# Kernel optimization log

Hardware: AMD Instinct MI355X
Metric: run time of the kernel (lower is better)

Reference implementation:

```python
import jax, jax.numpy as jnp
import numpy as np

# ---- static configuration (mirrors TimeFold init + deterministic prepare()) ----
B = 256
F = 512            # fft_length//2 + 1
T = 81             # input STFT frames
WIN = 1022         # window_length == frame_length == fft_length
HOP = 400          # hop_length
SEG = 1000         # segment_length
OVL = 50           # overlap_length
TO_HOP = 100       # deterministic choice of randint(1, hop_size=100)
SIG_LEN = (T - 1) * HOP + WIN            # 33022, inverse_stft output length

# prepare(): t segments kept, gaps of TO_HOP deleted
_t = SIG_LEN // (SEG + TO_HOP)
if SIG_LEN % (SEG + TO_HOP) >= SEG:
    _t += 1                               # _t = 30
KEPT_LEN = _t * SEG                       # 30000
OUT_LEN = SEG + (_t - 1) * (SEG - OVL)    # 28550
NF = 1 + (OUT_LEN - WIN) // HOP           # 69 output STFT frames

# indices kept after deleting the to_hop gaps (complement of delete_indices)
KEEP_IDX = np.concatenate([k * (SEG + TO_HOP) + np.arange(SEG) for k in range(_t)])

# overlap-add blending coefficients (length KEPT_LEN), built exactly as in prepare()
_ramp_up = np.arange(1, OVL + 1, dtype=np.float32) / OVL
_ramp_dn = np.arange(OVL, 0, -1, dtype=np.float32) / OVL
COEFF_INC = np.pad(np.tile(np.pad(_ramp_up, (0, SEG - OVL)), _t - 1), (SEG - OVL, OVL))
COEFF_DEC = np.pad(np.tile(np.pad(_ramp_dn, (SEG - OVL, 0)), _t - 1), (0, SEG))
_c = np.tile(np.pad(np.ones(SEG - 2 * OVL, np.float32), (OVL, OVL)), _t - 2)
_c = np.pad(np.pad(_c, (OVL, 0)), (SEG - OVL, 0), constant_values=1.0)
_c = np.pad(np.pad(_c, (0, OVL)), (0, SEG - OVL), constant_values=1.0)
COEFF_CONST = _c.astype(np.float32)

# final_delete_indices: drop [k*SEG, k*SEG+OVL) for k = 1.._t-1
_mask = np.ones(KEPT_LEN, bool)
for k in range(1, _t):
    _mask[k * SEG:k * SEG + OVL] = False
FINAL_KEEP = np.nonzero(_mask)[0]         # length OUT_LEN

# gather index grids for framing (static)
ISTFT_IDX = np.arange(T)[:, None] * HOP + np.arange(WIN)[None, :]
STFT_IDX = np.arange(NF)[:, None] * HOP + np.arange(WIN)[None, :]


def _hann(n):
    # periodic Hann, matches tf.signal.hann_window(periodic=True)
    return (0.5 - 0.5 * jnp.cos(2.0 * jnp.pi * jnp.arange(n, dtype=jnp.float32) / n)).astype(jnp.float32)


def _synthesis_window():
    w = _hann(WIN)
    denom = w * w
    overlaps = -(-WIN // HOP)
    denom = jnp.pad(denom, (0, overlaps * HOP - WIN))
    denom = denom.reshape(overlaps, HOP).sum(axis=0)
    denom = jnp.tile(denom, overlaps)[:WIN]
    return w / denom


def setup_inputs() -> dict:
    key = jax.random.key(0)
    x = jax.random.normal(key, (B, F, T, 2), dtype=jnp.float32)
    return {"x": x}


def reference(x) -> jnp.ndarray:
    # x: [B, 512, T, 2] real/imag STFT
    stfts = jax.lax.complex(x[..., 0], x[..., 1])          # [B, F, T]
    frames = jnp.transpose(stfts, (0, 2, 1))               # [B, T, F]
    # inverse_stft: irfft each frame, apply synthesis window, overlap-add
    tf_frames = jnp.fft.irfft(frames, n=WIN, axis=-1)
    tf_frames = tf_frames * _synthesis_window()
    sig = jnp.zeros((x.shape[0], SIG_LEN), jnp.float32).at[:, ISTFT_IDX].add(tf_frames)
    # dynamic segment delete (gather of kept indices)
    kept = sig[:, KEEP_IDX]                                # [B, KEPT_LEN]
    # shifted copy: drop first OVL samples, zero-pad at end
    shifted = jnp.concatenate(
        [kept[:, OVL:], jnp.zeros((x.shape[0], OVL), jnp.float32)], axis=1)
    # weighted overlap-add blend
    out = (jnp.asarray(COEFF_CONST) + jnp.asarray(COEFF_DEC)) * kept \
        + jnp.asarray(COEFF_INC) * shifted
    out = out[:, FINAL_KEEP]                               # [B, OUT_LEN]
    # forward STFT (periodic Hann, no padding)
    fr = out[:, STFT_IDX] * _hann(WIN)
    S = jnp.fft.rfft(fr, n=WIN, axis=-1)                   # [B, NF, 512]
    S = jnp.transpose(S, (0, 2, 1))                        # [B, 512, NF]
    return jnp.stack([S.real, S.imag], axis=-1)            # [B, 512, NF, 2]
```

## Files before the change

kernel.cpp:

```cpp
#include <hip/hip_runtime.h>
#include <math.h>

typedef unsigned short u16;
typedef unsigned int u32;

#define B_   256
#define F_   512
#define T_   81
#define WIN_ 1022
#define HOP_ 400
#define NF_  69
#define OUT_LEN_ 28550
#define SEG_ 1000
#define OVL_ 50

#define MA_  20736
#define MB_  17664
#define K_   1024
#define NMA_TILES 162
#define NMB_TILES 138
#define NMA_PAD   168
#define NMB_PAD   144

#define SYNWIN_B   0u
#define HANN_B     4096u
#define BASA_B     8192u
#define BASB_B     (BASA_B + 2097152u)
#define ABUF_B     (BASB_B + 2097152u)
#define TF_B       (ABUF_B + 42467328u)
#define OUTF_B     (TF_B + 42467328u)
#define OUTF_STRIDE_ 28672

typedef __attribute__((ext_vector_type(8))) short bf8_t;
typedef __attribute__((ext_vector_type(4))) float f4_t;
typedef const __attribute__((address_space(1))) void* as1cv;
typedef __attribute__((address_space(3))) void* as3v;

__device__ __forceinline__ float b2f(u16 v) {
  u32 u = ((u32)v) << 16; float f; __builtin_memcpy(&f, &u, 4); return f;
}
__device__ __forceinline__ u16 f2b(float f) {
  u32 u; __builtin_memcpy(&u, &f, 4);
  return (u16)((u + 0x7fffu + ((u >> 16) & 1u)) >> 16);
}

__global__ __launch_bounds__(256) void k1_tables(float* __restrict__ ws) {
  int i = blockIdx.x * 256 + threadIdx.x;
  if (i >= WIN_) return;
  const float twopi_N = 6.283185307179586f / (float)WIN_;
  float w = 0.5f - 0.5f * cosf(twopi_N * (float)i);
  int j = i % HOP_;
  float a = 0.5f - 0.5f * cosf(twopi_N * (float)j);
  float b = 0.5f - 0.5f * cosf(twopi_N * (float)(j + 400));
  float d = a * a + b * b;
  if (j + 800 < WIN_) {
    float c = 0.5f - 0.5f * cosf(twopi_N * (float)(j + 800));
    d += c * c;
  }
  ((float*)((char*)ws + SYNWIN_B))[i] = w / d;
  ((float*)((char*)ws + HANN_B))[i]   = w;
}

__global__ __launch_bounds__(256) void gen_basisA(const float* __restrict__ synwin,
                                                  u16* __restrict__ BA) {
  int n = blockIdx.x;
  float scale = (n < WIN_) ? synwin[n] * (1.0f / (float)WIN_) : 0.f;
  for (int k = threadIdx.x; k < 512; k += 256) {
    int m = (k * n) % WIN_;
    float ang = 6.283185307179586f * (float)m / (float)WIN_;
    float s, c; __sincosf(ang, &s, &c);
    bool edge = (k == 0) || (k == 511);
    float ck = edge ? 1.f : 2.f;
    float re = scale * ck * c;
    float im = edge ? 0.f : -scale * ck * s;
    BA[(size_t)n * K_ + 2 * k]     = f2b(re);
    BA[(size_t)n * K_ + 2 * k + 1] = f2b(im);
  }
}

__global__ __launch_bounds__(256) void gen_basisB(const float* __restrict__ hann,
                                                  u16* __restrict__ BB) {
  int k = blockIdx.x;
  for (int w = threadIdx.x; w < K_; w += 256) {
    float re = 0.f, im = 0.f;
    if (w < WIN_) {
      int m = (k * w) % WIN_;
      float ang = 6.283185307179586f * (float)m / (float)WIN_;
      float s, c; __sincosf(ang, &s, &c);
      float h = hann[w];
      re = h * c; im = -h * s;
    }
    BB[(size_t)(2 * k)     * K_ + w] = f2b(re);
    BB[(size_t)(2 * k + 1) * K_ + w] = f2b(im);
  }
}

__global__ __launch_bounds__(256) void prep1(const float* __restrict__ x,
                                             u16* __restrict__ Abuf) {
  __shared__ float2 tile[32][33];
  int k0 = blockIdx.x * 32, t0 = blockIdx.y * 32, b = blockIdx.z;
  int c = threadIdx.x & 31, rr = threadIdx.x >> 5;
  const float2* xp = (const float2*)x;
#pragma unroll
  for (int i = 0; i < 4; ++i) {
    int k = k0 + rr + 8 * i, t = t0 + c;
    float2 v = make_float2(0.f, 0.f);
    if (t < T_) v = xp[(size_t)(b * F_ + k) * T_ + t];
    tile[rr + 8 * i][c] = v;
  }
  __syncthreads();
#pragma unroll
  for (int i = 0; i < 4; ++i) {
    int t = t0 + rr + 8 * i, kc = c;
    if (t < T_) {
      float2 v = tile[kc][rr + 8 * i];
      u32 packed = (u32)f2b(v.x) | ((u32)f2b(v.y) << 16);
      *(u32*)&Abuf[(size_t)(b * T_ + t) * K_ + 2 * (k0 + kc)] = packed;
    }
  }
}

template <int EPI>
__global__ __launch_bounds__(256) void gemm_bf16(const u16* __restrict__ A,
                                                 const u16* __restrict__ Bt,
                                                 void* __restrict__ Cout) {
  __shared__ u16 sA[8 * 512];
  __shared__ u16 sB[8 * 512];
  const int tid = threadIdx.x;
  const int lane = tid & 63, wv = tid >> 6;

  int id = blockIdx.x;
  int xcd = id & 7, slot = id >> 3;
  int mt = (slot >> 3) * 8 + xcd;
  int nt = slot & 7;
  const int nM = (EPI == 0) ? NMA_TILES : NMB_TILES;
  if (mt >= nM) return;
  const int bm = mt * 128, bn = nt * 128;

  const int fr = lane & 15, fq = lane >> 4;
  const int s0 = 2 * wv, s1 = s0 + 1;

  const u16 *pA0, *pA1;
  if (EPI == 0) {
    pA0 = A + (size_t)(bm + 16 * s0 + fr) * K_ + fq * 8;
    pA1 = A + (size_t)(bm + 16 * s1 + fr) * K_ + fq * 8;
  } else {
    int m0 = bm + 16 * s0 + fr;
    int b0 = m0 / NF_, f0 = m0 - b0 * NF_;
    pA0 = A + (size_t)b0 * OUTF_STRIDE_ + f0 * HOP_ + fq * 8;
    int m1 = m0 + 16;
    int b1 = m1 / NF_, f1 = m1 - b1 * NF_;
    pA1 = A + (size_t)b1 * OUTF_STRIDE_ + f1 * HOP_ + fq * 8;
  }
  const u16* pB0 = Bt + (size_t)(bn + 16 * s0 + fr) * K_ + fq * 8;
  const u16* pB1 = Bt + (size_t)(bn + 16 * s1 + fr) * K_ + fq * 8;

  u16* lA0 = sA + s0 * 512;
  u16* lA1 = sA + s1 * 512;
  u16* lB0 = sB + s0 * 512;
  u16* lB1 = sB + s1 * 512;

  f4_t acc[4][4];
#pragma unroll
  for (int i = 0; i < 4; ++i)
#pragma unroll
    for (int j = 0; j < 4; ++j) acc[i][j] = (f4_t){0.f, 0.f, 0.f, 0.f};

  const int wm4 = (wv >> 1) * 4, wn4 = (wv & 1) * 4;

  for (int k0 = 0; k0 < K_; k0 += 32) {
    __builtin_amdgcn_global_load_lds((as1cv)(const void*)(pA0 + k0), (as3v)lA0, 16, 0, 0);
    __builtin_amdgcn_global_load_lds((as1cv)(const void*)(pA1 + k0), (as3v)lA1, 16, 0, 0);
    __builtin_amdgcn_global_load_lds((as1cv)(const void*)(pB0 + k0), (as3v)lB0, 16, 0, 0);
    __builtin_amdgcn_global_load_lds((as1cv)(const void*)(pB1 + k0), (as3v)lB1, 16, 0, 0);
    __builtin_amdgcn_s_waitcnt(0x0f70);
    __syncthreads();

    bf8_t af[4], bq[4];
#pragma unroll
    for (int i = 0; i < 4; ++i)
      af[i] = *(const bf8_t*)&sA[(wm4 + i) * 512 + lane * 8];
#pragma unroll
    for (int j = 0; j < 4; ++j)
      bq[j] = *(const bf8_t*)&sB[(wn4 + j) * 512 + lane * 8];
#pragma unroll
    for (int i = 0; i < 4; ++i)
#pragma unroll
      for (int j = 0; j < 4; ++j)
        acc[i][j] = __builtin_amdgcn_mfma_f32_16x16x32_bf16(af[i], bq[j], acc[i][j], 0, 0, 0);
    __syncthreads();
  }

  const int wm = wm4 * 16, wn = wn4 * 16;
  if (EPI == 0) {
    u16* C = (u16*)Cout;
#pragma unroll
    for (int i = 0; i < 4; ++i)
#pragma unroll
      for (int j = 0; j < 4; ++j) {
        int colg = bn + wn + 16 * j + fr;
#pragma unroll
        for (int r = 0; r < 4; ++r) {
          int rowg = bm + wm + 16 * i + fq * 4 + r;
          C[(size_t)rowg * K_ + colg] = f2b(acc[i][j][r]);
        }
      }
  } else {
    float* out = (float*)Cout;
    float* ep = ((wv & 2) ? (float*)sB : (float*)sA) + (wv & 1) * 1024;
    for (int j = 0; j < 4; ++j) {
#pragma unroll
      for (int i = 0; i < 4; ++i)
#pragma unroll
        for (int r = 0; r < 4; ++r) {
          int row64 = 16 * i + fq * 4 + r;
          ep[row64 * 16 + fr] = acc[i][j][r];
        }
      __syncthreads();
      int m = bm + wm + lane;
      int b = m / NF_;
      int f = m - b * NF_;
      int colbase = bn + wn + 16 * j;
#pragma unroll
      for (int a = 0; a < 8; ++a) {
        int k = (colbase >> 1) + a;
        float2 v = make_float2(ep[lane * 16 + 2 * a], ep[lane * 16 + 2 * a + 1]);
        ((float2*)out)[((size_t)b * F_ + k) * NF_ + f] = v;
      }
      __syncthreads();
    }
  }
}

__device__ __forceinline__ float sigval(const u16* __restrict__ tfb, int i) {
  int t1 = i / HOP_; if (t1 > T_ - 1) t1 = T_ - 1;
  int t0 = (i >= WIN_) ? (i - (WIN_ - 1) + HOP_ - 1) / HOP_ : 0;
  float acc = 0.f;
  for (int t = t0; t <= t1; ++t)
    acc += b2f(tfb[(size_t)t * K_ + (i - t * HOP_)]);
  return acc;
}

__global__ __launch_bounds__(256) void k3_fold(const u16* __restrict__ tf,
                                               u16* __restrict__ outf) {
  int id = blockIdx.x * 256 + threadIdx.x;
  if (id >= B_ * OUT_LEN_) return;
  int b = id / OUT_LEN_;
  int p = id - b * OUT_LEN_;
  int s, r;
  if (p < SEG_) { s = 0; r = p; }
  else {
    int q = p - SEG_;
    s = q / (SEG_ - OVL_) + 1;
    r = OVL_ + (q - (s - 1) * (SEG_ - OVL_));
  }
  const u16* tfb = tf + (size_t)b * T_ * K_;
  float val;
  if (r >= SEG_ - OVL_ && s <= 28) {
    float dec = (float)(SEG_ - r) * (1.f / (float)OVL_);
    float inc = (float)(r - (SEG_ - OVL_ - 1)) * (1.f / (float)OVL_);
    float v1 = sigval(tfb, s * 1100 + r);
    float v2 = sigval(tfb, (s + 1) * 1100 + (r - (SEG_ - OVL_)));
    val = dec * v1 + inc * v2;
  } else {
    val = sigval(tfb, s * 1100 + r);
  }
  outf[(size_t)b * OUTF_STRIDE_ + p] = f2b(val);
}

extern "C" void kernel_launch(void* const* d_in, const int* in_sizes, int n_in,
                              void* d_out, int out_size, void* d_ws, size_t ws_size,
                              hipStream_t stream) {
  const float* x = (const float*)d_in[0];
  char* ws = (char*)d_ws;
  float* synwin = (float*)(ws + SYNWIN_B);
  float* hann   = (float*)(ws + HANN_B);
  u16* BA   = (u16*)(ws + BASA_B);
  u16* BB   = (u16*)(ws + BASB_B);
  u16* Abuf = (u16*)(ws + ABUF_B);
  u16* TF   = (u16*)(ws + TF_B);
  u16* outf = (u16*)(ws + OUTF_B);

  hipLaunchKernelGGL(k1_tables, dim3(4), dim3(256), 0, stream, (float*)ws);
  hipLaunchKernelGGL(gen_basisA, dim3(1024), dim3(256), 0, stream, synwin, BA);
  hipLaunchKernelGGL(gen_basisB, dim3(512), dim3(256), 0, stream, hann, BB);
  hipLaunchKernelGGL(prep1, dim3(16, 3, 256), dim3(256), 0, stream, x, Abuf);
  hipLaunchKernelGGL((gemm_bf16<0>), dim3(NMA_PAD * 8), dim3(256), 0, stream,
                     Abuf, BA, (void*)TF);
  int n3 = B_ * OUT_LEN_;
  hipLaunchKernelGGL(k3_fold, dim3((n3 + 255) / 256), dim3(256), 0, stream, TF, outf);
  hipLaunchKernelGGL((gemm_bf16<1>), dim3(NMB_PAD * 8), dim3(256), 0, stream,
                     outf, BB, (void*)d_out);
}
```

Measured before the change: 364.3 us.

## Double-buffer GEMM LDS tiles and fold window tables into basis kernels

The bf16 GEMM now uses two LDS buffers, prefetching the next k-slice via global_load_lds while computing MFMAs on the current one. This aims to hide global load latency behind compute. The separate window-table kernel is removed and the windows are computed inline in the basis generators, dropping one launch. There is no explicit vmcnt wait inside the loop before the barrier, so correctness depends on the compiler inserting one.

```diff
diff --git a/kernel.cpp b/kernel.cpp
--- a/kernel.cpp
+++ b/kernel.cpp
@@ -22,9 +22,7 @@
 #define NMA_PAD   168
 #define NMB_PAD   144
 
-#define SYNWIN_B   0u
-#define HANN_B     4096u
-#define BASA_B     8192u
+#define BASA_B     0u
 #define BASB_B     (BASA_B + 2097152u)
 #define ABUF_B     (BASB_B + 2097152u)
 #define TF_B       (ABUF_B + 42467328u)
@@ -44,30 +42,25 @@
   return (u16)((u + 0x7fffu + ((u >> 16) & 1u)) >> 16);
 }
 
-__global__ __launch_bounds__(256) void k1_tables(float* __restrict__ ws) {
-  int i = blockIdx.x * 256 + threadIdx.x;
-  if (i >= WIN_) return;
+__global__ __launch_bounds__(256) void gen_basisA(u16* __restrict__ BA) {
+  int n = blockIdx.x;
   const float twopi_N = 6.283185307179586f / (float)WIN_;
-  float w = 0.5f - 0.5f * cosf(twopi_N * (float)i);
-  int j = i % HOP_;
-  float a = 0.5f - 0.5f * cosf(twopi_N * (float)j);
-  float b = 0.5f - 0.5f * cosf(twopi_N * (float)(j + 400));
-  float d = a * a + b * b;
-  if (j + 800 < WIN_) {
-    float c = 0.5f - 0.5f * cosf(twopi_N * (float)(j + 800));
-    d += c * c;
-  }
-  ((float*)((char*)ws + SYNWIN_B))[i] = w / d;
-  ((float*)((char*)ws + HANN_B))[i]   = w;
-}
-
-__global__ __launch_bounds__(256) void gen_basisA(const float* __restrict__ synwin,
-                                                  u16* __restrict__ BA) {
-  int n = blockIdx.x;
-  float scale = (n < WIN_) ? synwin[n] * (1.0f / (float)WIN_) : 0.f;
+  float scale = 0.f;
+  if (n < WIN_) {
+    float w = 0.5f - 0.5f * cosf(twopi_N * (float)n);
+    int j = n % HOP_;
+    float a = 0.5f - 0.5f * cosf(twopi_N * (float)j);
+    float b = 0.5f - 0.5f * cosf(twopi_N * (float)(j + 400));
+    float d = a * a + b * b;
+    if (j + 800 < WIN_) {
+      float c2 = 0.5f - 0.5f * cosf(twopi_N * (float)(j + 800));
+      d += c2 * c2;
+    }
+    scale = (w / d) * (1.0f / (float)WIN_);
+  }
   for (int k = threadIdx.x; k < 512; k += 256) {
     int m = (k * n) % WIN_;
-    float ang = 6.283185307179586f * (float)m / (float)WIN_;
+    float ang = twopi_N * (float)m;
     float s, c; __sincosf(ang, &s, &c);
     bool edge = (k == 0) || (k == 511);
     float ck = edge ? 1.f : 2.f;
@@ -78,16 +71,16 @@
   }
 }
 
-__global__ __launch_bounds__(256) void gen_basisB(const float* __restrict__ hann,
-                                                  u16* __restrict__ BB) {
+__global__ __launch_bounds__(256) void gen_basisB(u16* __restrict__ BB) {
   int k = blockIdx.x;
+  const float twopi_N = 6.283185307179586f / (float)WIN_;
   for (int w = threadIdx.x; w < K_; w += 256) {
     float re = 0.f, im = 0.f;
     if (w < WIN_) {
       int m = (k * w) % WIN_;
-      float ang = 6.283185307179586f * (float)m / (float)WIN_;
+      float ang = twopi_N * (float)m;
       float s, c; __sincosf(ang, &s, &c);
-      float h = hann[w];
+      float h = 0.5f - 0.5f * cosf(twopi_N * (float)w);
       re = h * c; im = -h * s;
     }
     BB[(size_t)(2 * k)     * K_ + w] = f2b(re);
@@ -124,8 +117,8 @@
 __global__ __launch_bounds__(256) void gemm_bf16(const u16* __restrict__ A,
                                                  const u16* __restrict__ Bt,
                                                  void* __restrict__ Cout) {
-  __shared__ u16 sA[8 * 512];
-  __shared__ u16 sB[8 * 512];
+  __shared__ u16 sA[2][4096];
+  __shared__ u16 sB[2][4096];
   const int tid = threadIdx.x;
   const int lane = tid & 63, wv = tid >> 6;
 
@@ -155,11 +148,6 @@
   const u16* pB0 = Bt + (size_t)(bn + 16 * s0 + fr) * K_ + fq * 8;
   const u16* pB1 = Bt + (size_t)(bn + 16 * s1 + fr) * K_ + fq * 8;
 
-  u16* lA0 = sA + s0 * 512;
-  u16* lA1 = sA + s1 * 512;
-  u16* lB0 = sB + s0 * 512;
-  u16* lB1 = sB + s1 * 512;
-
   f4_t acc[4][4];
 #pragma unroll
   for (int i = 0; i < 4; ++i)
@@ -168,27 +156,42 @@
 
   const int wm4 = (wv >> 1) * 4, wn4 = (wv & 1) * 4;
 
+  __builtin_amdgcn_global_load_lds((as1cv)(const void*)pA0, (as3v)(sA[0] + s0 * 512), 16, 0, 0);
+  __builtin_amdgcn_global_load_lds((as1cv)(const void*)pA1, (as3v)(sA[0] + s1 * 512), 16, 0, 0);
+  __builtin_amdgcn_global_load_lds((as1cv)(const void*)pB0, (as3v)(sB[0] + s0 * 512), 16, 0, 0);
+  __builtin_amdgcn_global_load_lds((as1cv)(const void*)pB1, (as3v)(sB[0] + s1 * 512), 16, 0, 0);
+  __builtin_amdgcn_s_waitcnt(0x0f70);
+  __syncthreads();
+
+  int cur = 0;
   for (int k0 = 0; k0 < K_; k0 += 32) {
-    __builtin_amdgcn_global_load_lds((as1cv)(const void*)(pA0 + k0), (as3v)lA0, 16, 0, 0);
-    __builtin_amdgcn_global_load_lds((as1cv)(const void*)(pA1 + k0), (as3v)lA1, 16, 0, 0);
-    __builtin_amdgcn_global_load_lds((as1cv)(const void*)(pB0 + k0), (as3v)lB0, 16, 0, 0);
-    __builtin_amdgcn_global_load_lds((as1cv)(const void*)(pB1 + k0), (as3v)lB1, 16, 0, 0);
-    __builtin_amdgcn_s_waitcnt(0x0f70);
-    __syncthreads();
-
+    int nxt = k0 + 32;
+    if (nxt < K_) {
+      u16* dA = sA[cur ^ 1];
+      u16* dB = sB[cur ^ 1];
+      __builtin_amdgcn_global_load_lds((as1cv)(const void*)(pA0 + nxt), (as3v)(dA + s0 * 512), 16, 0, 0);
+      __builtin_amdgcn_global_load_lds((as1cv)(const void*)(pA1 + nxt), (as3v)(dA + s1 * 512), 16, 0, 0);
+      __builtin_amdgcn_global_load_lds((as1cv)(const void*)(pB0 + nxt), (as3v)(dB + s0 * 512), 16, 0, 0);
+      __builtin_amdgcn_global_load_lds((as1cv)(const void*)(pB1 + nxt), (as3v)(dB + s1 * 512), 16, 0, 0);
+    }
+
+    const u16* cA = sA[cur];
+    const u16* cB = sB[cur];
     bf8_t af[4], bq[4];
 #pragma unroll
     for (int i = 0; i < 4; ++i)
-      af[i] = *(const bf8_t*)&sA[(wm4 + i) * 512 + lane * 8];
+      af[i] = *(const bf8_t*)&cA[(wm4 + i) * 512 + lane * 8];
 #pragma unroll
     for (int j = 0; j < 4; ++j)
-      bq[j] = *(const bf8_t*)&sB[(wn4 + j) * 512 + lane * 8];
+      bq[j] = *(const bf8_t*)&cB[(wn4 + j) * 512 + lane * 8];
 #pragma unroll
     for (int i = 0; i < 4; ++i)
 #pragma unroll
       for (int j = 0; j < 4; ++j)
         acc[i][j] = __builtin_amdgcn_mfma_f32_16x16x32_bf16(af[i], bq[j], acc[i][j], 0, 0, 0);
+
     __syncthreads();
+    cur ^= 1;
   }
 
   const int wm = wm4 * 16, wn = wn4 * 16;
@@ -207,7 +210,7 @@
       }
   } else {
     float* out = (float*)Cout;
-    float* ep = ((wv & 2) ? (float*)sB : (float*)sA) + (wv & 1) * 1024;
+    float* ep = ((wv & 2) ? (float*)sB[0] : (float*)sA[0]) + (wv & 1) * 1024;
     for (int j = 0; j < 4; ++j) {
 #pragma unroll
       for (int i = 0; i < 4; ++i)
@@ -273,17 +276,14 @@
                               hipStream_t stream) {
   const float* x = (const float*)d_in[0];
   char* ws = (char*)d_ws;
-  float* synwin = (float*)(ws + SYNWIN_B);
-  float* hann   = (float*)(ws + HANN_B);
   u16* BA   = (u16*)(ws + BASA_B);
   u16* BB   = (u16*)(ws + BASB_B);
   u16* Abuf = (u16*)(ws + ABUF_B);
   u16* TF   = (u16*)(ws + TF_B);
   u16* outf = (u16*)(ws + OUTF_B);
 
-  hipLaunchKernelGGL(k1_tables, dim3(4), dim3(256), 0, stream, (float*)ws);
-  hipLaunchKernelGGL(gen_basisA, dim3(1024), dim3(256), 0, stream, synwin, BA);
-  hipLaunchKernelGGL(gen_basisB, dim3(512), dim3(256), 0, stream, hann, BB);
+  hipLaunchKernelGGL(gen_basisA, dim3(1024), dim3(256), 0, stream, BA);
+  hipLaunchKernelGGL(gen_basisB, dim3(512), dim3(256), 0, stream, BB);
   hipLaunchKernelGGL(prep1, dim3(16, 3, 256), dim3(256), 0, stream, x, Abuf);
   hipLaunchKernelGGL((gemm_bf16<0>), dim3(NMA_PAD * 8), dim3(256), 0, stream,
                      Abuf, BA, (void*)TF);
```

Result: faster. 333.0 us (-8.6%).
